# Kernel optimization log

Hardware: AMD Instinct MI355X
Metric: run time of the kernel (lower is better)

Reference implementation:

```python
import math
import jax, jax.numpy as jnp
import numpy as np

B, S, HID = 2, 2048, 4096
H, KV = 32, 8
D = HID // H  # 128


def setup_inputs() -> dict:
    key = jax.random.key(0)
    ks = jax.random.split(key, 6)
    std = 0.02
    x = jax.random.normal(ks[0], (B, S, HID), dtype=jnp.float32)
    # causal additive mask, broadcast over batch and heads
    neg = jnp.full((S, S), -1e9, dtype=jnp.float32)
    mask = jnp.triu(neg, k=1)[None, None, :, :]
    q_w = jax.random.normal(ks[1], (HID, HID), dtype=jnp.float32) * std
    k_w = jax.random.normal(ks[2], (KV * D, HID), dtype=jnp.float32) * std
    v_w = jax.random.normal(ks[3], (KV * D, HID), dtype=jnp.float32) * std
    o_w = jax.random.normal(ks[4], (HID, HID), dtype=jnp.float32) * std
    return {
        "x": x, "mask": mask,
        "q_w": q_w, "q_b": jnp.zeros((HID,), jnp.float32),
        "k_w": k_w, "k_b": jnp.zeros((KV * D,), jnp.float32),
        "v_w": v_w, "v_b": jnp.zeros((KV * D,), jnp.float32),
        "o_w": o_w, "o_b": jnp.zeros((HID,), jnp.float32),
    }


def reference(x, mask, q_w, q_b, k_w, k_b, v_w, v_b, o_w, o_b):
    b, s, _ = x.shape
    rep = H // KV
    # projections (torch Linear convention: y = x @ W^T + b)
    q = (x @ q_w.T + q_b).reshape(b, s, H, D)
    k = (x @ k_w.T + k_b).reshape(b, s, KV, D)
    v = (x @ v_w.T + v_b).reshape(b, s, KV, D)
    # GQA kv-head repeat via concat: q head i attends to kv head (i mod KV)
    k = jnp.concatenate([k] * rep, axis=2)  # [b, s, H, D]
    v = jnp.concatenate([v] * rep, axis=2)
    # [b, H, s, D]
    q = q.transpose(0, 2, 1, 3)
    k = k.transpose(0, 2, 1, 3)
    v = v.transpose(0, 2, 1, 3)
    scores = jnp.einsum("bhqd,bhkd->bhqk", q, k) / math.sqrt(D)
    scores = scores + mask
    w = jax.nn.softmax(scores, axis=-1)
    attn = jnp.einsum("bhqk,bhkd->bhqd", w, v)
    attn = attn.transpose(0, 2, 1, 3).reshape(b, s, HID)
    return attn @ o_w.T + o_b
```

## Files before the change

### kernel.cpp

```cpp
#include <hip/hip_runtime.h>
#include <hip/hip_bf16.h>
#include <cstdint>

typedef __attribute__((ext_vector_type(8))) short s8vec;
typedef __attribute__((ext_vector_type(4))) float f4vec;

#define DEV __device__ __forceinline__

constexpr int Bn = 2, Sn = 2048, HIDn = 4096, Hn = 32, KVn = 8, Dn = 128;

typedef const __attribute__((address_space(1))) void gvoid_t;
typedef __attribute__((address_space(3))) void lvoid_t;

DEV void async_ld16(const void* g, void* l) {
  __builtin_amdgcn_global_load_lds((gvoid_t*)g, (lvoid_t*)l, 16, 0, 0);
}

DEV f4vec mfma16(s8vec a, s8vec b, f4vec c) {
  return __builtin_amdgcn_mfma_f32_16x16x32_bf16(a, b, c, 0, 0, 0);
}

__global__ void cvt_all(const float* __restrict__ x, const float* __restrict__ qw,
                        const float* __restrict__ kw, const float* __restrict__ vw,
                        const float* __restrict__ ow,
                        __hip_bfloat16* __restrict__ xb, __hip_bfloat16* __restrict__ qwb,
                        __hip_bfloat16* __restrict__ kwb, __hip_bfloat16* __restrict__ vwb,
                        __hip_bfloat16* __restrict__ owb) {
  const int i = blockIdx.x * 256 + threadIdx.x;
  const float* src; __hip_bfloat16* dst; int off;
  if (i < 4194304)       { src = x;  dst = xb;  off = i; }
  else if (i < 8388608)  { src = qw; dst = qwb; off = i - 4194304; }
  else if (i < 9437184)  { src = kw; dst = kwb; off = i - 8388608; }
  else if (i < 10485760) { src = vw; dst = vwb; off = i - 9437184; }
  else                   { src = ow; dst = owb; off = i - 10485760; }
  float4 f = ((const float4*)src)[off];
  union { __hip_bfloat16 h[4]; uint2 u; } cv;
  cv.h[0] = __float2bfloat16(f.x);
  cv.h[1] = __float2bfloat16(f.y);
  cv.h[2] = __float2bfloat16(f.z);
  cv.h[3] = __float2bfloat16(f.w);
  ((uint2*)dst)[off] = cv.u;
}

template <typename EpiF>
DEV void gemm_bt_body(const __hip_bfloat16* A, const __hip_bfloat16* Bw, int K,
                      long m0, long n0, EpiF epi) {
  __shared__ __hip_bfloat16 As[3][256 * 64];
  __shared__ __hip_bfloat16 Bs[3][128 * 64];
  const int t = threadIdx.x;
  const int w = t >> 6, l = t & 63;
  const int lane15 = l & 15, quad = l >> 4;
  const int wm = (w >> 1) << 6;
  const int wn = (w & 1) << 6;

  f4vec acc[4][4] = {};

  const int col_e = ((l & 7) << 3) ^ (((l >> 5) & 1) << 4);
  const __hip_bfloat16* agA = A + (m0 + w * 8 + (l >> 3)) * (long)K + col_e;
  const __hip_bfloat16* agB = Bw + (n0 + w * 8 + (l >> 3)) * (long)K + col_e;
  const long rowK64 = (long)K << 6;

  auto stageA = [&](int buf, int kt, int i) {
    async_ld16(agA + (long)i * rowK64 + ((long)kt << 6),
               (char*)(As[buf]) + ((i * 8 + w) << 10));
  };
  auto stageB = [&](int buf, int kt, int i) {
    async_ld16(agB + (long)i * rowK64 + ((long)kt << 6),
               (char*)(Bs[buf]) + ((i * 8 + w) << 10));
  };

  const int colxor = (lane15 & 4) << 3;
  const int cq = (quad << 4) ^ colxor;
  int arow[4], brow[4];
#pragma unroll
  for (int i = 0; i < 4; i++) arow[i] = (wm + i * 16 + lane15) << 7;
#pragma unroll
  for (int j = 0; j < 4; j++) brow[j] = (wn + j * 16 + lane15) << 7;

  const int NT = K >> 6;

#pragma unroll
  for (int i = 0; i < 4; i++) stageA(0, 0, i);
#pragma unroll
  for (int i = 0; i < 2; i++) stageB(0, 0, i);
#pragma unroll
  for (int i = 0; i < 4; i++) stageA(1, 1, i);
#pragma unroll
  for (int i = 0; i < 2; i++) stageB(1, 1, i);
  asm volatile("s_waitcnt vmcnt(6)" ::: "memory");
  __builtin_amdgcn_s_barrier();
  __builtin_amdgcn_sched_barrier(0);

  int bi = 0, nb = 2;
  for (int tau = 0; tau < NT; ++tau) {
    const char* Ab = (const char*)As[bi];
    const char* Bb = (const char*)Bs[bi];
    const bool st = (tau + 2) < NT;
    s8vec af[4], bf4[4];

#pragma unroll
    for (int i = 0; i < 4; i++) af[i] = *(const s8vec*)(Ab + arow[i] + cq);
#pragma unroll
    for (int j = 0; j < 4; j++) bf4[j] = *(const s8vec*)(Bb + brow[j] + cq);
    if (st) { stageA(nb, tau + 2, 0); stageA(nb, tau + 2, 1); stageB(nb, tau + 2, 0); }
    __builtin_amdgcn_s_setprio(1);
#pragma unroll
    for (int i = 0; i < 4; i++)
#pragma unroll
      for (int j = 0; j < 4; j++) acc[i][j] = mfma16(af[i], bf4[j], acc[i][j]);
    __builtin_amdgcn_s_setprio(0);

#pragma unroll
    for (int i = 0; i < 4; i++) af[i] = *(const s8vec*)(Ab + arow[i] + cq + 64);
#pragma unroll
    for (int j = 0; j < 4; j++) bf4[j] = *(const s8vec*)(Bb + brow[j] + cq + 64);
    if (st) { stageA(nb, tau + 2, 2); stageA(nb, tau + 2, 3); stageB(nb, tau + 2, 1); }
    __builtin_amdgcn_s_setprio(1);
#pragma unroll
    for (int i = 0; i < 4; i++)
#pragma unroll
      for (int j = 0; j < 4; j++) acc[i][j] = mfma16(af[i], bf4[j], acc[i][j]);
    __builtin_amdgcn_s_setprio(0);

    if (tau + 1 < NT) {
      if (st) asm volatile("s_waitcnt vmcnt(6)" ::: "memory");
      else    asm volatile("s_waitcnt vmcnt(0)" ::: "memory");
      __builtin_amdgcn_s_barrier();
      __builtin_amdgcn_sched_barrier(0);
    }
    bi = (bi + 1 == 3) ? 0 : bi + 1;
    nb = (nb + 1 == 3) ? 0 : nb + 1;
  }
  epi(acc, wm, wn, lane15, quad);
}

__launch_bounds__(512, 2)
__global__ void gemm_qkv(const __hip_bfloat16* __restrict__ xb,
                         const __hip_bfloat16* __restrict__ qwb,
                         const __hip_bfloat16* __restrict__ kwb,
                         const __hip_bfloat16* __restrict__ vwb,
                         const float* __restrict__ qb, const float* __restrict__ kb,
                         const float* __restrict__ vb,
                         __hip_bfloat16* __restrict__ qh, __hip_bfloat16* __restrict__ kh,
                         __hip_bfloat16* __restrict__ vth) {
  const int bx = blockIdx.x;
  const long m0 = (long)blockIdx.y << 8;
  int mode; long n0;
  const __hip_bfloat16* Bw; const float* bias;
  if (bx < 32)      { mode = 0; Bw = qwb; bias = qb; n0 = (long)bx << 7; }
  else if (bx < 40) { mode = 1; Bw = kwb; bias = kb; n0 = (long)(bx - 32) << 7; }
  else              { mode = 2; Bw = vwb; bias = vb; n0 = (long)(bx - 40) << 7; }

  gemm_bt_body(xb, Bw, 4096, m0, n0,
    [&](f4vec (&acc)[4][4], int wm, int wn, int lane15, int quad) {
      float bv[4];
#pragma unroll
      for (int j = 0; j < 4; j++) bv[j] = bias[n0 + wn + j * 16 + lane15];
#pragma unroll
      for (int i = 0; i < 4; i++)
#pragma unroll
        for (int j = 0; j < 4; j++)
#pragma unroll
          for (int r = 0; r < 4; r++) {
            const long gm = m0 + wm + i * 16 + (quad << 2) + r;
            const long gn = n0 + wn + j * 16 + lane15;
            const float v = acc[i][j][r] + bv[j];
            const long bb = gm >> 11, ss = gm & 2047;
            const long hh = gn >> 7, dd = gn & 127;
            const __hip_bfloat16 hv = __float2bfloat16(v);
            if (mode == 0)
              qh[(((bb * Hn + hh) * Sn + ss) << 7) + dd] = hv;
            else if (mode == 1)
              kh[(((bb * KVn + hh) * Sn + ss) << 7) + dd] = hv;
            else
              vth[((bb * KVn + hh) * Dn + dd) * (long)Sn + ss] = hv;
          }
    });
}

__launch_bounds__(512, 2)
__global__ void gemm_out(const __hip_bfloat16* __restrict__ A,
                         const __hip_bfloat16* __restrict__ Bw,
                         const float* __restrict__ bias, float* __restrict__ Cout) {
  const long m0 = (long)blockIdx.y << 8;
  const long n0 = (long)blockIdx.x << 7;
  gemm_bt_body(A, Bw, 4096, m0, n0,
    [&](f4vec (&acc)[4][4], int wm, int wn, int lane15, int quad) {
      float bv[4];
#pragma unroll
      for (int j = 0; j < 4; j++) bv[j] = bias[n0 + wn + j * 16 + lane15];
#pragma unroll
      for (int i = 0; i < 4; i++)
#pragma unroll
        for (int j = 0; j < 4; j++)
#pragma unroll
          for (int r = 0; r < 4; r++) {
            const long gm = m0 + wm + i * 16 + (quad << 2) + r;
            const long gn = n0 + wn + j * 16 + lane15;
            Cout[gm * HIDn + gn] = acc[i][j][r] + bv[j];
          }
    });
}

__launch_bounds__(256, 2)
__global__ void attn_fused(const __hip_bfloat16* __restrict__ Qh,
                           const __hip_bfloat16* __restrict__ Kh,
                           const __hip_bfloat16* __restrict__ Vt,
                           __hip_bfloat16* __restrict__ Oa) {
  __shared__ __hip_bfloat16 Ks[2][64 * 128];
  __shared__ __hip_bfloat16 Vs[2][128 * 64];
  __shared__ __hip_bfloat16 Ps[4][32 * 64];

  const int pair = blockIdx.x;
  const int h = blockIdx.y;
  const int b = blockIdx.z;
  const int kv = h & 7;

  const int t = threadIdx.x, w = t >> 6, l = t & 63;
  const int lane15 = l & 15, quad = l >> 4;
  const int swz = lane15 & 7;

  const char* KgB = (const char*)(Kh + ((long)(b * KVn + kv)) * Sn * Dn);
  const char* VgB = (const char*)(Vt + ((long)(b * KVn + kv)) * Dn * (long)Sn);

  const int kc = (t & 15) ^ ((t >> 4) & 7);
  const char* kg_base = KgB + (t >> 4) * 256 + kc * 16;
  const int vc = (t & 7) ^ ((t >> 3) & 7);
  const char* vg_base = VgB + (t >> 3) * (size_t)(Sn * 2) + vc * 16;

  const short* Psh = (const short*)Ps[w];
  short* Psw = (short*)Ps[w];
  const float cscale = 0.08838834764831845f * 1.4426950408889634f;
  const float coff = -8.0f * 1.4426950408889634f;

  for (int ph = 0; ph < 2; ph++) {
    const int qt = ph ? (15 - pair) : pair;

    s8vec aq[2][4];
    {
      const short* Qgs = (const short*)(Qh + (((long)(b * Hn + h)) * Sn + qt * 128) * (long)Dn);
#pragma unroll
      for (int i = 0; i < 2; i++)
#pragma unroll
        for (int kk = 0; kk < 4; kk++)
          aq[i][kk] = *(const s8vec*)(Qgs + (w * 32 + i * 16 + lane15) * 128 + kk * 32 + (quad << 3));
    }
    float lsum[2][4] = {};
    f4vec acco[2][8] = {};

    __syncthreads();
    {
      char* lk = (char*)Ks[0] + (w << 10);
      char* lv = (char*)Vs[0] + (w << 10);
#pragma unroll
      for (int i = 0; i < 4; i++) async_ld16(kg_base + i * 4096, lk + i * 4096);
#pragma unroll
      for (int i = 0; i < 4; i++) async_ld16(vg_base + (size_t)i * 32 * Sn * 2, lv + i * 4096);
    }

    const int n_kt = 2 * qt + 2, full_kt = 2 * qt;
    for (int kt = 0; kt < n_kt; kt++) {
      const int cur = kt & 1;
      __syncthreads();
      if (kt + 1 < n_kt) {
        char* lk = (char*)Ks[cur ^ 1] + (w << 10);
        char* lv = (char*)Vs[cur ^ 1] + (w << 10);
        const char* kg = kg_base + (size_t)(kt + 1) * 16384;
        const char* vg = vg_base + (size_t)(kt + 1) * 128;
#pragma unroll
        for (int i = 0; i < 4; i++) async_ld16(kg + i * 4096, lk + i * 4096);
#pragma unroll
        for (int i = 0; i < 4; i++) async_ld16(vg + (size_t)i * 32 * Sn * 2, lv + i * 4096);
      }
      const short* Ksh = (const short*)Ks[cur];
      const short* Vsh = (const short*)Vs[cur];
      const bool need_mask = (kt >= full_kt);

#pragma unroll
      for (int j = 0; j < 4; j++) {
        f4vec as0 = {}, as1 = {};
#pragma unroll
        for (int kk = 0; kk < 4; kk++) {
          const s8vec bk = *(const s8vec*)(Ksh + (j * 16 + lane15) * 128 + (((quad + 4 * kk) ^ swz) << 3));
          as0 = mfma16(aq[0][kk], bk, as0);
          as1 = mfma16(aq[1][kk], bk, as1);
        }
        const int pc = j * 16 + lane15;
        const int kcol = kt * 64 + pc;
#pragma unroll
        for (int i = 0; i < 2; i++) {
#pragma unroll
          for (int r = 0; r < 4; r++) {
            const int pr = i * 16 + (quad << 2) + r;
            float sv = (i ? as1[r] : as0[r]) * cscale + coff;
            if (need_mask) {
              const int qr = qt * 128 + w * 32 + pr;
              if (kcol > qr) sv = -1000000.0f;
            }
            const float p = __builtin_amdgcn_exp2f(sv);
            lsum[i][r] += p;
            Psw[pr * 64 + ((((pc >> 3) ^ (pr & 7)) << 3) | (pc & 7))] =
                __bfloat16_as_short(__float2bfloat16(p));
          }
        }
      }
      asm volatile("s_waitcnt lgkmcnt(0)" ::: "memory");

#pragma unroll
      for (int kk = 0; kk < 2; kk++) {
        s8vec ap[2], bv8[8];
#pragma unroll
        for (int i = 0; i < 2; i++)
          ap[i] = *(const s8vec*)(Psh + (i * 16 + lane15) * 64 + (((quad + 4 * kk) ^ swz) << 3));
#pragma unroll
        for (int j = 0; j < 8; j++)
          bv8[j] = *(const s8vec*)(Vsh + (j * 16 + lane15) * 64 + (((quad + 4 * kk) ^ swz) << 3));
#pragma unroll
        for (int i = 0; i < 2; i++)
#pragma unroll
          for (int j = 0; j < 8; j++)
            acco[i][j] = mfma16(ap[i], bv8[j], acco[i][j]);
      }
    }

#pragma unroll
    for (int i = 0; i < 2; i++)
#pragma unroll
      for (int r = 0; r < 4; r++) {
        float s = lsum[i][r];
#pragma unroll
        for (int d = 1; d < 16; d <<= 1) s += __shfl_xor(s, d);
        lsum[i][r] = 1.0f / s;
      }
#pragma unroll
    for (int i = 0; i < 2; i++) {
#pragma unroll
      for (int r = 0; r < 4; r++) {
        const int row = qt * 128 + w * 32 + i * 16 + (quad << 2) + r;
        const long base = ((long)b * Sn + row) * HIDn + h * Dn;
#pragma unroll
        for (int j = 0; j < 8; j++)
          Oa[base + j * 16 + lane15] = __float2bfloat16(acco[i][j][r] * lsum[i][r]);
      }
    }
  }
}

extern "C" void kernel_launch(void* const* d_in, const int* in_sizes, int n_in,
                              void* d_out, int out_size, void* d_ws, size_t ws_size,
                              hipStream_t stream) {
  const float* x   = (const float*)d_in[0];
  const float* q_w = (const float*)d_in[2];
  const float* q_b = (const float*)d_in[3];
  const float* k_w = (const float*)d_in[4];
  const float* k_b = (const float*)d_in[5];
  const float* v_w = (const float*)d_in[6];
  const float* v_b = (const float*)d_in[7];
  const float* o_w = (const float*)d_in[8];
  const float* o_b = (const float*)d_in[9];

  char* ws = (char*)d_ws;
  size_t off = 0;
  auto nxt = [&](size_t bytes) { char* p = ws + off; off += bytes; return p; };
  __hip_bfloat16* xb  = (__hip_bfloat16*)nxt(33554432);
  __hip_bfloat16* qwb = (__hip_bfloat16*)nxt(33554432);
  __hip_bfloat16* kwb = (__hip_bfloat16*)nxt(8388608);
  __hip_bfloat16* vwb = (__hip_bfloat16*)nxt(8388608);
  __hip_bfloat16* owb = (__hip_bfloat16*)nxt(33554432);
  __hip_bfloat16* qh  = (__hip_bfloat16*)nxt(33554432);
  __hip_bfloat16* kh  = (__hip_bfloat16*)nxt(8388608);
  __hip_bfloat16* vth = (__hip_bfloat16*)nxt(8388608);
  __hip_bfloat16* at  = (__hip_bfloat16*)nxt(33554432);
  (void)ws_size; (void)in_sizes; (void)n_in; (void)out_size;

  cvt_all<<<57344, 256, 0, stream>>>(x, q_w, k_w, v_w, o_w, xb, qwb, kwb, vwb, owb);
  gemm_qkv<<<dim3(48, 16), 512, 0, stream>>>(xb, qwb, kwb, vwb, q_b, k_b, v_b, qh, kh, vth);
  attn_fused<<<dim3(8, 32, 2), 256, 0, stream>>>(qh, kh, vth, at);
  gemm_out<<<dim3(32, 16), 512, 0, stream>>>(at, owb, o_b, (float*)d_out);
}
```

Baseline: 728.3 us.

## Enlarge GEMM tiles to 256x256 with double-buffered LDS and new swizzle

The shared GEMM body moves from 256x128 block tiles with a triple-buffered pipeline to 256x256 tiles with a double buffer. Each wave now owns a 128x64 output subtile, and all fragments for both k-halves are loaded up front. The next stage is issued mid-iteration, after a barrier that protects the reused buffer. The LDS XOR swizzle changes and occupancy drops to one block per CU. The aim is more arithmetic intensity per LDS/global load, at the cost of higher register pressure, fewer blocks (384 and 256) across the CUs, and less latency hiding.

New measurement: 719.6 us. About the same (-1.2%).

```diff
diff --git a/kernel.cpp b/kernel.cpp
--- a/kernel.cpp
+++ b/kernel.cpp
@@ -45,96 +45,88 @@
 template <typename EpiF>
 DEV void gemm_bt_body(const __hip_bfloat16* A, const __hip_bfloat16* Bw, int K,
                       long m0, long n0, EpiF epi) {
-  __shared__ __hip_bfloat16 As[3][256 * 64];
-  __shared__ __hip_bfloat16 Bs[3][128 * 64];
+  __shared__ __hip_bfloat16 As[2][256 * 64];
+  __shared__ __hip_bfloat16 Bs[2][256 * 64];
   const int t = threadIdx.x;
   const int w = t >> 6, l = t & 63;
   const int lane15 = l & 15, quad = l >> 4;
-  const int wm = (w >> 1) << 6;
-  const int wn = (w & 1) << 6;
-
-  f4vec acc[4][4] = {};
-
-  const int col_e = ((l & 7) << 3) ^ (((l >> 5) & 1) << 4);
-  const __hip_bfloat16* agA = A + (m0 + w * 8 + (l >> 3)) * (long)K + col_e;
-  const __hip_bfloat16* agB = Bw + (n0 + w * 8 + (l >> 3)) * (long)K + col_e;
-  const long rowK64 = (long)K << 6;
-
-  auto stageA = [&](int buf, int kt, int i) {
-    async_ld16(agA + (long)i * rowK64 + ((long)kt << 6),
-               (char*)(As[buf]) + ((i * 8 + w) << 10));
+  const int wm = (w >> 2) << 7;
+  const int wn = (w & 3) << 6;
+
+  f4vec acc[8][4] = {};
+
+  const int srow = w * 8 + (l >> 3);
+  const int scol = ((l & 7) ^ (l >> 3)) << 3;
+  const __hip_bfloat16* gA = A + (m0 + srow) * (long)K + scol;
+  const __hip_bfloat16* gB = Bw + (n0 + srow) * (long)K + scol;
+  const long i64K = (long)K << 6;
+
+  auto stage = [&](int buf, int kt) {
+    char* la = (char*)As[buf] + (w << 10);
+    char* lb = (char*)Bs[buf] + (w << 10);
+    const long ko = (long)kt << 6;
+#pragma unroll
+    for (int i = 0; i < 4; i++) async_ld16(gA + (long)i * i64K + ko, la + i * 8192);
+#pragma unroll
+    for (int i = 0; i < 4; i++) async_ld16(gB + (long)i * i64K + ko, lb + i * 8192);
   };
-  auto stageB = [&](int buf, int kt, int i) {
-    async_ld16(agB + (long)i * rowK64 + ((long)kt << 6),
-               (char*)(Bs[buf]) + ((i * 8 + w) << 10));
-  };
-
-  const int colxor = (lane15 & 4) << 3;
-  const int cq = (quad << 4) ^ colxor;
-  int arow[4], brow[4];
-#pragma unroll
-  for (int i = 0; i < 4; i++) arow[i] = (wm + i * 16 + lane15) << 7;
-#pragma unroll
-  for (int j = 0; j < 4; j++) brow[j] = (wn + j * 16 + lane15) << 7;
+
+  const int arA = (wm + lane15) << 7;
+  const int arB = (wn + lane15) << 7;
+  const int c0 = (quad << 4) ^ ((lane15 & 7) << 4);
+  const int c1 = c0 ^ 64;
 
   const int NT = K >> 6;
 
-#pragma unroll
-  for (int i = 0; i < 4; i++) stageA(0, 0, i);
-#pragma unroll
-  for (int i = 0; i < 2; i++) stageB(0, 0, i);
-#pragma unroll
-  for (int i = 0; i < 4; i++) stageA(1, 1, i);
-#pragma unroll
-  for (int i = 0; i < 2; i++) stageB(1, 1, i);
-  asm volatile("s_waitcnt vmcnt(6)" ::: "memory");
+  stage(0, 0);
+  stage(1, 1);
+  asm volatile("s_waitcnt vmcnt(8)" ::: "memory");
   __builtin_amdgcn_s_barrier();
   __builtin_amdgcn_sched_barrier(0);
 
-  int bi = 0, nb = 2;
   for (int tau = 0; tau < NT; ++tau) {
-    const char* Ab = (const char*)As[bi];
-    const char* Bb = (const char*)Bs[bi];
-    const bool st = (tau + 2) < NT;
-    s8vec af[4], bf4[4];
-
-#pragma unroll
-    for (int i = 0; i < 4; i++) af[i] = *(const s8vec*)(Ab + arow[i] + cq);
-#pragma unroll
-    for (int j = 0; j < 4; j++) bf4[j] = *(const s8vec*)(Bb + brow[j] + cq);
-    if (st) { stageA(nb, tau + 2, 0); stageA(nb, tau + 2, 1); stageB(nb, tau + 2, 0); }
+    const int cur = tau & 1;
+    const char* Ab = (const char*)As[cur];
+    const char* Bb = (const char*)Bs[cur];
+    s8vec af0[8], af1[8], bf0[4], bf1[4];
+#pragma unroll
+    for (int i = 0; i < 8; i++) {
+      af0[i] = *(const s8vec*)(Ab + arA + i * 2048 + c0);
+      af1[i] = *(const s8vec*)(Ab + arA + i * 2048 + c1);
+    }
+#pragma unroll
+    for (int j = 0; j < 4; j++) {
+      bf0[j] = *(const s8vec*)(Bb + arB + j * 2048 + c0);
+      bf1[j] = *(const s8vec*)(Bb + arB + j * 2048 + c1);
+    }
     __builtin_amdgcn_s_setprio(1);
 #pragma unroll
-    for (int i = 0; i < 4; i++)
-#pragma unroll
-      for (int j = 0; j < 4; j++) acc[i][j] = mfma16(af[i], bf4[j], acc[i][j]);
+    for (int i = 0; i < 8; i++)
+#pragma unroll
+      for (int j = 0; j < 4; j++) acc[i][j] = mfma16(af0[i], bf0[j], acc[i][j]);
     __builtin_amdgcn_s_setprio(0);
-
-#pragma unroll
-    for (int i = 0; i < 4; i++) af[i] = *(const s8vec*)(Ab + arow[i] + cq + 64);
-#pragma unroll
-    for (int j = 0; j < 4; j++) bf4[j] = *(const s8vec*)(Bb + brow[j] + cq + 64);
-    if (st) { stageA(nb, tau + 2, 2); stageA(nb, tau + 2, 3); stageB(nb, tau + 2, 1); }
+    __builtin_amdgcn_sched_barrier(0);
+    asm volatile("s_waitcnt lgkmcnt(0)" ::: "memory");
+    __builtin_amdgcn_sched_barrier(0);
+    __builtin_amdgcn_s_barrier();
+    if (tau + 2 < NT) stage(cur, tau + 2);
     __builtin_amdgcn_s_setprio(1);
 #pragma unroll
-    for (int i = 0; i < 4; i++)
-#pragma unroll
-      for (int j = 0; j < 4; j++) acc[i][j] = mfma16(af[i], bf4[j], acc[i][j]);
+    for (int i = 0; i < 8; i++)
+#pragma unroll
+      for (int j = 0; j < 4; j++) acc[i][j] = mfma16(af1[i], bf1[j], acc[i][j]);
     __builtin_amdgcn_s_setprio(0);
-
     if (tau + 1 < NT) {
-      if (st) asm volatile("s_waitcnt vmcnt(6)" ::: "memory");
-      else    asm volatile("s_waitcnt vmcnt(0)" ::: "memory");
+      if (tau + 2 < NT) asm volatile("s_waitcnt vmcnt(8)" ::: "memory");
+      else              asm volatile("s_waitcnt vmcnt(0)" ::: "memory");
       __builtin_amdgcn_s_barrier();
       __builtin_amdgcn_sched_barrier(0);
     }
-    bi = (bi + 1 == 3) ? 0 : bi + 1;
-    nb = (nb + 1 == 3) ? 0 : nb + 1;
   }
   epi(acc, wm, wn, lane15, quad);
 }
 
-__launch_bounds__(512, 2)
+__launch_bounds__(512, 1)
 __global__ void gemm_qkv(const __hip_bfloat16* __restrict__ xb,
                          const __hip_bfloat16* __restrict__ qwb,
                          const __hip_bfloat16* __restrict__ kwb,
@@ -147,17 +139,17 @@
   const long m0 = (long)blockIdx.y << 8;
   int mode; long n0;
   const __hip_bfloat16* Bw; const float* bias;
-  if (bx < 32)      { mode = 0; Bw = qwb; bias = qb; n0 = (long)bx << 7; }
-  else if (bx < 40) { mode = 1; Bw = kwb; bias = kb; n0 = (long)(bx - 32) << 7; }
-  else              { mode = 2; Bw = vwb; bias = vb; n0 = (long)(bx - 40) << 7; }
+  if (bx < 16)      { mode = 0; Bw = qwb; bias = qb; n0 = (long)bx << 8; }
+  else if (bx < 20) { mode = 1; Bw = kwb; bias = kb; n0 = (long)(bx - 16) << 8; }
+  else              { mode = 2; Bw = vwb; bias = vb; n0 = (long)(bx - 20) << 8; }
 
   gemm_bt_body(xb, Bw, 4096, m0, n0,
-    [&](f4vec (&acc)[4][4], int wm, int wn, int lane15, int quad) {
+    [&](f4vec (&acc)[8][4], int wm, int wn, int lane15, int quad) {
       float bv[4];
 #pragma unroll
       for (int j = 0; j < 4; j++) bv[j] = bias[n0 + wn + j * 16 + lane15];
 #pragma unroll
-      for (int i = 0; i < 4; i++)
+      for (int i = 0; i < 8; i++)
 #pragma unroll
         for (int j = 0; j < 4; j++)
 #pragma unroll
@@ -178,19 +170,19 @@
     });
 }
 
-__launch_bounds__(512, 2)
+__launch_bounds__(512, 1)
 __global__ void gemm_out(const __hip_bfloat16* __restrict__ A,
                          const __hip_bfloat16* __restrict__ Bw,
                          const float* __restrict__ bias, float* __restrict__ Cout) {
   const long m0 = (long)blockIdx.y << 8;
-  const long n0 = (long)blockIdx.x << 7;
+  const long n0 = (long)blockIdx.x << 8;
   gemm_bt_body(A, Bw, 4096, m0, n0,
-    [&](f4vec (&acc)[4][4], int wm, int wn, int lane15, int quad) {
+    [&](f4vec (&acc)[8][4], int wm, int wn, int lane15, int quad) {
       float bv[4];
 #pragma unroll
       for (int j = 0; j < 4; j++) bv[j] = bias[n0 + wn + j * 16 + lane15];
 #pragma unroll
-      for (int i = 0; i < 4; i++)
+      for (int i = 0; i < 8; i++)
 #pragma unroll
         for (int j = 0; j < 4; j++)
 #pragma unroll
@@ -374,7 +366,7 @@
   (void)ws_size; (void)in_sizes; (void)n_in; (void)out_size;
 
   cvt_all<<<57344, 256, 0, stream>>>(x, q_w, k_w, v_w, o_w, xb, qwb, kwb, vwb, owb);
-  gemm_qkv<<<dim3(48, 16), 512, 0, stream>>>(xb, qwb, kwb, vwb, q_b, k_b, v_b, qh, kh, vth);
+  gemm_qkv<<<dim3(24, 16), 512, 0, stream>>>(xb, qwb, kwb, vwb, q_b, k_b, v_b, qh, kh, vth);
   attn_fused<<<dim3(8, 32, 2), 256, 0, stream>>>(qh, kh, vth, at);
-  gemm_out<<<dim3(32, 16), 512, 0, stream>>>(at, owb, o_b, (float*)d_out);
-}
+  gemm_out<<<dim3(16, 16), 512, 0, stream>>>(at, owb, o_b, (float*)d_out);
+}
```
